# Performance work log

Measured on AMD Instinct MI355X. Metric: run time of the kernel, lower is better.

Reference implementation:

```python
import jax, jax.numpy as jnp
import numpy as np

N_NODES = 50000
N_EDGES = 800000
N_GRAPHS = 1024
N_PAIRS = 16384
N_CL = 16
IN_CH = 64
EMB = 128
HID = 256
OUT = 1


def _xavier(key, shape):
    fan_in, fan_out = shape[-2], shape[-1]
    lim = (6.0 / (fan_in + fan_out)) ** 0.5
    return jax.random.uniform(key, shape, jnp.float32, -lim, lim)


def setup_inputs() -> dict:
    key = jax.random.key(0)
    ks = jax.random.split(key, 12)
    x = jax.random.normal(ks[0], (N_NODES, IN_CH), jnp.float32)
    edge_index = jax.random.randint(ks[1], (2, N_EDGES), 0, N_NODES)
    batch = jnp.sort(jax.random.randint(ks[2], (N_NODES,), 0, N_GRAPHS))
    drug_drug_batch = jax.random.randint(ks[3], (2, N_PAIRS), 0, N_GRAPHS)
    edge_cell_lines = jax.random.randint(ks[4], (N_PAIRS,), 0, N_CL)
    conv1_w = _xavier(ks[5], (IN_CH, EMB))
    conv2_w = _xavier(ks[6], (EMB, EMB))
    reg_w1 = _xavier(ks[7], (N_CL, 2 * EMB, HID))
    reg_w2 = _xavier(ks[8], (N_CL, HID, OUT))
    return dict(
        x=x,
        conv1_w=conv1_w, conv1_b=jnp.zeros((EMB,), jnp.float32),
        conv2_w=conv2_w, conv2_b=jnp.zeros((EMB,), jnp.float32),
        reg_w1=reg_w1, reg_b1=jnp.zeros((N_CL, HID), jnp.float32),
        reg_w2=reg_w2, reg_b2=jnp.zeros((N_CL, OUT), jnp.float32),
        edge_index=edge_index, batch=batch,
        drug_drug_batch=drug_drug_batch, edge_cell_lines=edge_cell_lines,
    )


def _forward(x, conv1_w, conv1_b, conv2_w, conv2_b,
             reg_w1, reg_b1, reg_w2, reg_b2,
             edge_index, batch, drug_drug_batch, edge_cell_lines):
    n = x.shape[0]
    # GCN normalization with self-loops (PyG GCNConv default)
    loop = jnp.arange(n)
    row = jnp.concatenate([edge_index[0], loop])  # source
    col = jnp.concatenate([edge_index[1], loop])  # target
    deg = jax.ops.segment_sum(jnp.ones(row.shape[0], x.dtype), col, num_segments=n)
    dinv = jnp.where(deg > 0, jax.lax.rsqrt(deg), 0.0)
    norm = dinv[row] * dinv[col]  # [E+N]

    def gcn(h, W, b):
        hw = h @ W
        agg = jax.ops.segment_sum(norm[:, None] * hw[row], col, num_segments=n)
        return agg + b

    h = jax.nn.relu(gcn(x, conv1_w, conv1_b))
    h = jax.nn.relu(gcn(h, conv2_w, conv2_b))

    # scatter-mean pooling over graphs
    gsum = jax.ops.segment_sum(h, batch, num_segments=N_GRAPHS)
    cnt = jax.ops.segment_sum(jnp.ones(n, h.dtype), batch, num_segments=N_GRAPHS)
    graph_embeds = gsum / jnp.maximum(cnt, 1.0)[:, None]

    # np.digitize(ddb, unique(ddb)+1); with contiguous ids 0..G-1 this is identity,
    # expressed faithfully via searchsorted against bins = arange(G)+1
    bins = jnp.arange(N_GRAPHS) + 1
    q = jnp.searchsorted(bins, drug_drug_batch, side='right')
    pair = jnp.concatenate([graph_embeds[q[0]], graph_embeds[q[1]]], axis=1)  # [P, 2*EMB]

    # per-cell-line Linear-ReLU-Linear, computed for all lines then selected
    hcl = jax.nn.relu(jnp.einsum('pe,ceh->pch', pair, reg_w1) + reg_b1[None])  # [P,C,H]
    ocl = jnp.einsum('pch,cho->pco', hcl, reg_w2) + reg_b2[None]               # [P,C,O]
    preds = jnp.take_along_axis(ocl, edge_cell_lines[:, None, None], axis=1)[:, 0, :]
    return preds


def reference(x, conv1_w, conv1_b, conv2_w, conv2_b,
              reg_w1, reg_b1, reg_w2, reg_b2,
              edge_index, batch, drug_drug_batch, edge_cell_lines):
    return _forward(x, conv1_w, conv1_b, conv2_w, conv2_b,
                    reg_w1, reg_b1, reg_w2, reg_b2,
                    edge_index, batch, drug_drug_batch, edge_cell_lines)
```

## Files before the change

kernel.cpp:

```cpp
#include <hip/hip_runtime.h>
#include <hip/hip_fp16.h>

#define NN 50000
#define NE 800000
#define NG 1024
#define NP 16384
#define NCL 16
#define INCH 64
#define EMB 128
#define HID 256

#define NB 391
#define NCHUNK 400
#define EPB 2000

#define CDIV(a,b) (((a)+(b)-1)/(b))

typedef _Float16 f16x8 __attribute__((ext_vector_type(8)));
typedef float    f32x4 __attribute__((ext_vector_type(4)));

template<int NW>
__device__ __forceinline__ int block_excl_scan(int v, int t, int* incl_out) {
    int lane = t & 63, w = t >> 6;
    int s = v;
#pragma unroll
    for (int d = 1; d < 64; d <<= 1) {
        int u = __shfl_up(s, d, 64);
        if (lane >= d) s += u;
    }
    __shared__ int wsum[NW];
    if (lane == 63) wsum[w] = s;
    __syncthreads();
    int add = 0;
    for (int k = 0; k < w; ++k) add += wsum[k];
    *incl_out = s + add;
    return s + add - v;
}

__global__ __launch_bounds__(256) void k_cnt(const int* __restrict__ cols,
                                             int* __restrict__ cnt) {
    __shared__ int hist[NB];
    int ch = blockIdx.x, t = threadIdx.x;
    for (int b = t; b < NB; b += 256) hist[b] = 0;
    __syncthreads();
    for (int e = ch * EPB + t; e < (ch + 1) * EPB; e += 256)
        atomicAdd(&hist[cols[e] >> 7], 1);
    __syncthreads();
    for (int b = t; b < NB; b += 256) cnt[b * NCHUNK + ch] = hist[b];
}

__global__ __launch_bounds__(512) void k_bscan(int* __restrict__ cnt,
                                               int* __restrict__ btot) {
    int b = blockIdx.x, t = threadIdx.x;
    int v = (t < NCHUNK) ? cnt[b * NCHUNK + t] : 0;
    int incl;
    int excl = block_excl_scan<8>(v, t, &incl);
    if (t < NCHUNK) cnt[b * NCHUNK + t] = excl;
    if (t == NCHUNK - 1) btot[b] = incl;
}

__global__ __launch_bounds__(512) void k_btot(const int* __restrict__ btot,
                                              int* __restrict__ bbase) {
    int t = threadIdx.x;
    int v = (t < NB) ? btot[t] : 0;
    int incl;
    int excl = block_excl_scan<8>(v, t, &incl);
    if (t < NB) bbase[t] = excl;
    if (t == NB - 1) bbase[NB] = incl;
}

__global__ __launch_bounds__(256) void k_part(const int* __restrict__ rows,
                                              const int* __restrict__ cols,
                                              const int* __restrict__ cnt,
                                              const int* __restrict__ bbase,
                                              int* __restrict__ ebuf) {
    __shared__ int cur[NB];
    int ch = blockIdx.x, t = threadIdx.x;
    for (int b = t; b < NB; b += 256) cur[b] = bbase[b] + cnt[b * NCHUNK + ch];
    __syncthreads();
    for (int e = ch * EPB + t; e < (ch + 1) * EPB; e += 256) {
        int c = cols[e], r = rows[e];
        int pos = atomicAdd(&cur[c >> 7], 1);
        ebuf[pos] = (r << 7) | (c & 127);
    }
}

__global__ __launch_bounds__(256) void k_bsort(const int* __restrict__ ebuf,
                                               const int* __restrict__ bbase,
                                               const float* __restrict__ x,
                                               int* __restrict__ off,
                                               float* __restrict__ dinv,
                                               int* __restrict__ srows,
                                               __half* __restrict__ xs) {
    __shared__ int   ldeg[128];
    __shared__ int   lcur[128];
    __shared__ float ldinv[128];
    int b = blockIdx.x, t = threadIdx.x;
    int n0 = b << 7;
    int nloc = min(128, NN - n0);
    int beg = bbase[b], end = bbase[b + 1];
    if (t < 128) ldeg[t] = 0;
    __syncthreads();
    for (int i = beg + t; i < end; i += 256)
        atomicAdd(&ldeg[ebuf[i] & 127], 1);
    __syncthreads();
    int v = (t < nloc) ? ldeg[t] : 0;
    int incl;
    int excl = block_excl_scan<4>(v, t, &incl);
    if (t < nloc) {
        off[n0 + t]  = beg + excl + v;
        float d = rsqrtf((float)(v + 1));
        dinv[n0 + t] = d;
        ldinv[t] = d;
        lcur[t] = beg + excl;
    }
    __syncthreads();
    for (int i = beg + t; i < end; i += 256) {
        int e = ebuf[i];
        int pos = atomicAdd(&lcur[e & 127], 1);
        srows[pos] = e >> 7;
    }
    const float4* Xx = (const float4*)x;
#pragma unroll
    for (int i = 0; i < 8; ++i) {
        int f4 = t + i * 256;
        int rloc = f4 >> 4, kq = f4 & 15;
        if (rloc < nloc) {
            float d = ldinv[rloc];
            float4 vv = Xx[(size_t)(n0 + rloc) * 16 + kq];
            __half2 h[2];
            h[0] = __floats2half2_rn(d * vv.x, d * vv.y);
            h[1] = __floats2half2_rn(d * vv.z, d * vv.w);
            ((float2*)xs)[(size_t)(n0 + rloc) * 16 + kq] = *(float2*)h;
        }
    }
}

__global__ __launch_bounds__(256) void k_wconv(const float* __restrict__ W,
                                               __half* __restrict__ WT, int K) {
    int i = blockIdx.x * 256 + threadIdx.x;
    if (i >= K * 128) return;
    int k = i >> 7, n = i & 127;
    WT[n * K + k] = __float2half(W[i]);
}

template<int FEAT, bool ZB>
__global__ __launch_bounds__(256) void k_gath_h(const int* __restrict__ off,
                                                const int* __restrict__ srows,
                                                const float* __restrict__ dinv,
                                                const __half* __restrict__ SRC,
                                                __half* __restrict__ DST,
                                                float* __restrict__ zbuf) {
    if (ZB) {
        if (blockIdx.x < 512) zbuf[(blockIdx.x << 8) + threadIdx.x] = 0.f;
    }
    constexpr int NC = FEAT / 8;
    constexpr int PL = NC / 8;
    int node = blockIdx.x * 4 + (threadIdx.x >> 6);
    int lane = threadIdx.x & 63;
    int slot = lane >> 3, q = lane & 7;
    if (node >= NN) return;
    int beg = node ? off[node - 1] : 0;
    int end = off[node];
    float di = dinv[node];
    const float4* S4 = (const float4*)SRC;

    float acc[PL][8];
#pragma unroll
    for (int i = 0; i < PL; ++i)
#pragma unroll
        for (int j = 0; j < 8; ++j) acc[i][j] = 0.f;

    if (slot == 0) {
#pragma unroll
        for (int i = 0; i < PL; ++i) {
            float4 raw = S4[node * NC + i * 8 + q];
            const __half2* h = (const __half2*)&raw;
#pragma unroll
            for (int j = 0; j < 4; ++j) {
                float2 f = __half22float2(h[j]);
                acc[i][2 * j + 0] = f.x;
                acc[i][2 * j + 1] = f.y;
            }
        }
    }
    for (int e = beg + slot; e < end; e += 8) {
        int r = srows[e];
#pragma unroll
        for (int i = 0; i < PL; ++i) {
            float4 raw = S4[r * NC + i * 8 + q];
            const __half2* h = (const __half2*)&raw;
#pragma unroll
            for (int j = 0; j < 4; ++j) {
                float2 f = __half22float2(h[j]);
                acc[i][2 * j + 0] += f.x;
                acc[i][2 * j + 1] += f.y;
            }
        }
    }
#pragma unroll
    for (int d = 8; d < 64; d <<= 1)
#pragma unroll
        for (int i = 0; i < PL; ++i)
#pragma unroll
            for (int j = 0; j < 8; ++j)
                acc[i][j] += __shfl_xor(acc[i][j], d, 64);

    if (lane < 8) {
        float4* D4 = (float4*)DST;
#pragma unroll
        for (int i = 0; i < PL; ++i) {
            float4 pk;
            __half2* hp = (__half2*)&pk;
            hp[0] = __floats2half2_rn(di * acc[i][0], di * acc[i][1]);
            hp[1] = __floats2half2_rn(di * acc[i][2], di * acc[i][3]);
            hp[2] = __floats2half2_rn(di * acc[i][4], di * acc[i][5]);
            hp[3] = __floats2half2_rn(di * acc[i][6], di * acc[i][7]);
            D4[node * NC + i * 8 + lane] = pk;
        }
    }
}

template<int K, bool RS, bool POOL>
__global__ __launch_bounds__(256) void gemm_mf(const __half* __restrict__ X,
                                               const __half* __restrict__ WT,
                                               const float* __restrict__ bias,
                                               const float* __restrict__ rs,
                                               const int* __restrict__ batch,
                                               float* __restrict__ Y, int M) {
    constexpr int KP = K + 8;
    __shared__ __half Xs[64 * KP];
    __shared__ __half Ws[128 * KP];
    __shared__ int sb[64];
    const int t = threadIdx.x;
    const int row0 = blockIdx.x * 64;

    const float4* X8 = (const float4*)X;
#pragma unroll
    for (int i = t; i < 64 * (K / 8); i += 256) {
        int r = i / (K / 8), ch = i % (K / 8);
        float4 v = make_float4(0.f, 0.f, 0.f, 0.f);
        if (row0 + r < M) v = X8[(size_t)(row0 + r) * (K / 8) + ch];
        *(float4*)&Xs[r * KP + ch * 8] = v;
    }
    const float4* W8 = (const float4*)WT;
#pragma unroll
    for (int i = t; i < 128 * (K / 8); i += 256) {
        int n = i / (K / 8), ch = i % (K / 8);
        *(float4*)&Ws[n * KP + ch * 8] = W8[i];
    }
    if (POOL) {
        if (t < 64) sb[t] = (row0 + t < M) ? batch[row0 + t] : -1;
    }
    __syncthreads();

    const int w  = t >> 6;
    const int l  = t & 63;
    const int lm = l & 15, lg = l >> 4;

    f32x4 acc[8];
#pragma unroll
    for (int c = 0; c < 8; ++c) acc[c] = (f32x4){0.f, 0.f, 0.f, 0.f};

#pragma unroll
    for (int kk = 0; kk < K / 32; ++kk) {
        f16x8 a = *(const f16x8*)&Xs[(16 * w + lm) * KP + kk * 32 + lg * 8];
#pragma unroll
        for (int c = 0; c < 8; ++c) {
            f16x8 bf = *(const f16x8*)&Ws[(16 * c + lm) * KP + kk * 32 + lg * 8];
            acc[c] = __builtin_amdgcn_mfma_f32_16x16x32_f16(a, bf, acc[c], 0, 0, 0);
        }
    }

    float bcol[8];
#pragma unroll
    for (int c = 0; c < 8; ++c) bcol[c] = bias[16 * c + lm];

    if (POOL) {
#pragma unroll
        for (int c = 0; c < 8; ++c) {
            int rung = -1;
            float run = 0.f;
#pragma unroll
            for (int j = 0; j < 4; ++j) {
                int rr = 16 * w + 4 * lg + j;
                int g = (row0 + rr < M) ? sb[rr] : -1;
                if (g != rung) {
                    if (rung >= 0) atomicAdd(&Y[rung * 128 + 16 * c + lm], run);
                    run = 0.f;
                    rung = g;
                }
                if (g >= 0) run += fmaxf(acc[c][j] + bcol[c], 0.f);
            }
            if (rung >= 0) atomicAdd(&Y[rung * 128 + 16 * c + lm], run);
        }
        return;
    }

    __half* Yh = (__half*)Y;
#pragma unroll
    for (int j = 0; j < 4; ++j) {
        int r = row0 + 16 * w + 4 * lg + j;
        if (r < M) {
            float d = RS ? rs[r] : 1.f;
#pragma unroll
            for (int c = 0; c < 8; ++c) {
                float v = d * fmaxf(acc[c][j] + bcol[c], 0.f);
                Yh[(size_t)r * 128 + 16 * c + lm] = __float2half(v);
            }
        }
    }
}

__global__ __launch_bounds__(128) void k_div(float* __restrict__ gsum,
                                             const int* __restrict__ batch) {
    int g = blockIdx.x;
    __shared__ float inv;
    if (threadIdx.x == 0) {
        int lo = 0, hi = NN;
        while (lo < hi) { int m = (lo + hi) >> 1; if (batch[m] < g) lo = m + 1; else hi = m; }
        int s = lo;
        lo = 0; hi = NN;
        while (lo < hi) { int m = (lo + hi) >> 1; if (batch[m] < g + 1) lo = m + 1; else hi = m; }
        float c = (float)(lo - s);
        inv = 1.f / fmaxf(c, 1.f);
    }
    __syncthreads();
    gsum[g * 128 + threadIdx.x] *= inv;
}

__global__ __launch_bounds__(256) void gemm_bat(const float* __restrict__ GE,
                                                const float* __restrict__ W1,
                                                float* __restrict__ Aarr,
                                                float* __restrict__ Barr) {
    __shared__ float Xt[32][132];
    __shared__ float Wsh[32][128];
    const int t  = threadIdx.x;
    const int tr = t >> 4;
    const int tc = t & 15;
    const int row0 = blockIdx.x * 128;
    const int y = blockIdx.y;
    const int z = blockIdx.z;
    const int lrow = t & 127;
    const int khalf = t >> 7;

    const float* Wbase = W1 + (z >> 1) * (HID * HID) + (z & 1) * (128 * HID) + y * 128;

    float acc[8][8];
#pragma unroll
    for (int i = 0; i < 8; ++i)
#pragma unroll
        for (int j = 0; j < 8; ++j) acc[i][j] = 0.f;

    const float4* X4 = (const float4*)GE;

    for (int k0 = 0; k0 < 128; k0 += 32) {
        __syncthreads();
#pragma unroll
        for (int q = 0; q < 4; ++q) {
            int kq = 4 * khalf + q;
            float4 xv = X4[(row0 + lrow) * 32 + (k0 >> 2) + kq];
            Xt[4 * kq + 0][lrow] = xv.x;
            Xt[4 * kq + 1][lrow] = xv.y;
            Xt[4 * kq + 2][lrow] = xv.z;
            Xt[4 * kq + 3][lrow] = xv.w;
        }
        const float4* Wc4 = (const float4*)(Wbase + k0 * HID);
#pragma unroll
        for (int i = 0; i < 4; ++i) {
            int f4 = t + i * 256;
            int k = f4 >> 5, c4 = f4 & 31;
            ((float4*)&Wsh[k][0])[c4] = Wc4[k * 64 + c4];
        }
        __syncthreads();
#pragma unroll 2
        for (int k = 0; k < 32; ++k) {
            float xf[8], wf[8];
            *(float4*)&xf[0] = *(const float4*)&Xt[k][8 * tr];
            *(float4*)&xf[4] = *(const float4*)&Xt[k][8 * tr + 4];
            *(float4*)&wf[0] = *(const float4*)&Wsh[k][8 * tc];
            *(float4*)&wf[4] = *(const float4*)&Wsh[k][8 * tc + 4];
#pragma unroll
            for (int i = 0; i < 8; ++i)
#pragma unroll
                for (int j = 0; j < 8; ++j)
                    acc[i][j] = fmaf(xf[i], wf[j], acc[i][j]);
        }
    }
    float* Obase = (z & 1) ? Barr : Aarr;
    float4* O4 = (float4*)Obase;
#pragma unroll
    for (int i = 0; i < 8; ++i) {
        int g = row0 + 8 * tr + i;
        size_t base = ((size_t)((z >> 1) * NG + g) * HID + y * 128 + 8 * tc) >> 2;
        O4[base + 0] = make_float4(acc[i][0], acc[i][1], acc[i][2], acc[i][3]);
        O4[base + 1] = make_float4(acc[i][4], acc[i][5], acc[i][6], acc[i][7]);
    }
}

__global__ __launch_bounds__(256) void k_pair(const float* __restrict__ Aarr,
                                              const float* __restrict__ Barr,
                                              const int* __restrict__ ddb,
                                              const int* __restrict__ ecl,
                                              const float* __restrict__ B1,
                                              const float* __restrict__ W2,
                                              const float* __restrict__ B2,
                                              float* __restrict__ out) {
    int p = blockIdx.x * 4 + (threadIdx.x >> 6);
    int lane = threadIdx.x & 63;
    int c = ecl[p];
    int a = ddb[p];
    int b = ddb[NP + p];
    const float4* rA = (const float4*)&Aarr[((size_t)c * NG + a) * HID];
    const float4* rB = (const float4*)&Barr[((size_t)c * NG + b) * HID];
    const float4* b1 = (const float4*)&B1[c * HID];
    const float4* w2 = (const float4*)&W2[c * HID];
    float4 va = rA[lane], vb = rB[lane], v1 = b1[lane], v2 = w2[lane];
    float hx = va.x + vb.x + v1.x;
    float hy = va.y + vb.y + v1.y;
    float hz = va.z + vb.z + v1.z;
    float hw = va.w + vb.w + v1.w;
    float s = 0.f;
    s = fmaf(hx > 0.f ? hx : 0.f, v2.x, s);
    s = fmaf(hy > 0.f ? hy : 0.f, v2.y, s);
    s = fmaf(hz > 0.f ? hz : 0.f, v2.z, s);
    s = fmaf(hw > 0.f ? hw : 0.f, v2.w, s);
    for (int o = 32; o; o >>= 1) s += __shfl_down(s, o, 64);
    if (lane == 0) out[p] = s + B2[c];
}

extern "C" void kernel_launch(void* const* d_in, const int* in_sizes, int n_in,
                              void* d_out, int out_size, void* d_ws, size_t ws_size,
                              hipStream_t stream) {
    const float* x    = (const float*)d_in[0];
    const float* c1w  = (const float*)d_in[1];
    const float* c1b  = (const float*)d_in[2];
    const float* c2w  = (const float*)d_in[3];
    const float* c2b  = (const float*)d_in[4];
    const float* rw1  = (const float*)d_in[5];
    const float* rb1  = (const float*)d_in[6];
    const float* rw2  = (const float*)d_in[7];
    const float* rb2  = (const float*)d_in[8];
    const int*   eidx = (const int*)d_in[9];
    const int*   batch= (const int*)d_in[10];
    const int*   ddb  = (const int*)d_in[11];
    const int*   ecl  = (const int*)d_in[12];
    float* out = (float*)d_out;

    int*   off   = (int*)d_ws;
    int*   srows = off + 50048;
    float* dinv  = (float*)(srows + NE);
    float* bufA  = dinv + 50048;
    float* bufB  = bufA + NN * EMB;

    int*    ebuf  = (int*)bufA;
    int*    cnt   = (int*)(bufB + 1700000);
    int*    btot  = cnt + NB * NCHUNK;
    int*    bbase = btot + 512;
    __half* xs    = (__half*)bufB;
    __half* aggXh = (__half*)bufA;
    __half* H1h   = (__half*)bufB;
    __half* aggHh = (__half*)bufA;
    float*  gsum  = bufA + 4500000;
    __half* w1t   = (__half*)(bufA + 4700000);
    __half* w2t   = (__half*)(bufA + 4710000);
    float*  Aarr  = bufA;
    float*  Barr  = bufB;

    const int* erow = eidx;
    const int* ecol = eidx + NE;

    k_wconv<<<CDIV(INCH*128,256),256,0,stream>>>(c1w, w1t, INCH);
    k_wconv<<<CDIV(EMB*128,256),256,0,stream>>>(c2w, w2t, EMB);

    k_cnt  <<<NCHUNK, 256, 0, stream>>>(ecol, cnt);
    k_bscan<<<NB,     512, 0, stream>>>(cnt, btot);
    k_btot <<<1,      512, 0, stream>>>(btot, bbase);
    k_part <<<NCHUNK, 256, 0, stream>>>(erow, ecol, cnt, bbase, ebuf);
    k_bsort<<<NB,     256, 0, stream>>>(ebuf, bbase, x, off, dinv, srows, xs);

    k_gath_h<INCH,true><<<CDIV(NN,4),256,0,stream>>>(off, srows, dinv, xs, aggXh, gsum);
    gemm_mf<INCH,true,false><<<CDIV(NN,64),256,0,stream>>>(aggXh, w1t, c1b, dinv, nullptr, (float*)H1h, NN);

    k_gath_h<EMB,false><<<CDIV(NN,4),256,0,stream>>>(off, srows, dinv, H1h, aggHh, nullptr);
    gemm_mf<EMB,false,true><<<CDIV(NN,64),256,0,stream>>>(aggHh, w2t, c2b, nullptr, batch, gsum, NN);
    k_div<<<NG,128,0,stream>>>(gsum, batch);

    dim3 bgrid(NG/128, 2, 2*NCL);
    gemm_bat<<<bgrid,256,0,stream>>>(gsum, rw1, Aarr, Barr);
    k_pair<<<NP/4,256,0,stream>>>(Aarr, Barr, ddb, ecl, rb1, rw2, rb2, out);
}
```

Before: 178.3 us.

## Move per-cell-line pair GEMM to fp16 MFMA with hi/lo split weights

Replaces the fp32 FMA batched GEMM (graph embeddings x regressor W1) with an MFMA 16x16x32 fp16 kernel. The weights are pre-split into hi and lo fp16 halves by a new conversion kernel and accumulated in two passes to recover precision. The graph-mean kernel now emits fp16 embeddings. Embeddings are rounded to fp16 without compensation, and an extra weight-conversion kernel runs on every call.

```diff
diff --git a/kernel.cpp b/kernel.cpp
--- a/kernel.cpp
+++ b/kernel.cpp
@@ -144,6 +144,25 @@
     WT[n * K + k] = __float2half(W[i]);
 }
 
+__global__ __launch_bounds__(256) void k_wconvb(const float* __restrict__ W1,
+                                                __half* __restrict__ Whl) {
+    int i = blockIdx.x * 256 + threadIdx.x;
+    if (i >= 32 * 256 * 16) return;
+    int ch = i & 15, tg = (i >> 4) & 255, z = i >> 12;
+    int c = z >> 1, part = z & 1;
+    f16x8 hi, lo;
+#pragma unroll
+    for (int j = 0; j < 8; ++j) {
+        float v = W1[(size_t)c * 65536 + (size_t)(part * 128 + ch * 8 + j) * 256 + tg];
+        _Float16 h = (_Float16)v;
+        hi[j] = h;
+        lo[j] = (_Float16)(v - (float)h);
+    }
+    size_t base = ((size_t)z * 256 + tg) * 16 + ch;
+    ((f16x8*)Whl)[base] = hi;
+    ((f16x8*)Whl)[(size_t)32 * 256 * 16 + base] = lo;
+}
+
 template<int FEAT, bool ZB>
 __global__ __launch_bounds__(256) void k_gath_h(const int* __restrict__ off,
                                                 const int* __restrict__ srows,
@@ -312,8 +331,9 @@
     }
 }
 
-__global__ __launch_bounds__(128) void k_div(float* __restrict__ gsum,
-                                             const int* __restrict__ batch) {
+__global__ __launch_bounds__(128) void k_div(const float* __restrict__ gsum,
+                                             const int* __restrict__ batch,
+                                             __half* __restrict__ geh) {
     int g = blockIdx.x;
     __shared__ float inv;
     if (threadIdx.x == 0) {
@@ -326,75 +346,65 @@
         inv = 1.f / fmaxf(c, 1.f);
     }
     __syncthreads();
-    gsum[g * 128 + threadIdx.x] *= inv;
-}
-
-__global__ __launch_bounds__(256) void gemm_bat(const float* __restrict__ GE,
-                                                const float* __restrict__ W1,
+    geh[g * 128 + threadIdx.x] = __float2half(gsum[g * 128 + threadIdx.x] * inv);
+}
+
+__global__ __launch_bounds__(256) void gemm_bat(const __half* __restrict__ GEh,
+                                                const __half* __restrict__ Whl,
                                                 float* __restrict__ Aarr,
                                                 float* __restrict__ Barr) {
-    __shared__ float Xt[32][132];
-    __shared__ float Wsh[32][128];
-    const int t  = threadIdx.x;
-    const int tr = t >> 4;
-    const int tc = t & 15;
-    const int row0 = blockIdx.x * 128;
-    const int y = blockIdx.y;
-    const int z = blockIdx.z;
-    const int lrow = t & 127;
-    const int khalf = t >> 7;
-
-    const float* Wbase = W1 + (z >> 1) * (HID * HID) + (z & 1) * (128 * HID) + y * 128;
-
-    float acc[8][8];
-#pragma unroll
-    for (int i = 0; i < 8; ++i)
-#pragma unroll
-        for (int j = 0; j < 8; ++j) acc[i][j] = 0.f;
-
-    const float4* X4 = (const float4*)GE;
-
-    for (int k0 = 0; k0 < 128; k0 += 32) {
+    constexpr int KP = 128 + 8;
+    __shared__ __half Xs[64 * KP];
+    __shared__ __half Ws[128 * KP];
+    const int t = threadIdx.x;
+    const int row0 = blockIdx.x * 64;
+    const int y = blockIdx.y, z = blockIdx.z;
+
+    const float4* X8 = (const float4*)GEh;
+#pragma unroll
+    for (int i = t; i < 64 * 16; i += 256) {
+        int r = i >> 4, ch = i & 15;
+        *(float4*)&Xs[r * KP + ch * 8] = X8[(size_t)(row0 + r) * 16 + ch];
+    }
+
+    const int w  = t >> 6;
+    const int l  = t & 63;
+    const int lm = l & 15, lg = l >> 4;
+
+    f32x4 acc[8];
+#pragma unroll
+    for (int c = 0; c < 8; ++c) acc[c] = (f32x4){0.f, 0.f, 0.f, 0.f};
+
+    const float4* W8 = (const float4*)Whl;
+#pragma unroll
+    for (int pass = 0; pass < 2; ++pass) {
         __syncthreads();
-#pragma unroll
-        for (int q = 0; q < 4; ++q) {
-            int kq = 4 * khalf + q;
-            float4 xv = X4[(row0 + lrow) * 32 + (k0 >> 2) + kq];
-            Xt[4 * kq + 0][lrow] = xv.x;
-            Xt[4 * kq + 1][lrow] = xv.y;
-            Xt[4 * kq + 2][lrow] = xv.z;
-            Xt[4 * kq + 3][lrow] = xv.w;
-        }
-        const float4* Wc4 = (const float4*)(Wbase + k0 * HID);
-#pragma unroll
-        for (int i = 0; i < 4; ++i) {
-            int f4 = t + i * 256;
-            int k = f4 >> 5, c4 = f4 & 31;
-            ((float4*)&Wsh[k][0])[c4] = Wc4[k * 64 + c4];
+        size_t wbase = ((size_t)pass * 32 + z) * 256 * 16;
+#pragma unroll
+        for (int i = t; i < 128 * 16; i += 256) {
+            int n = i >> 4, ch = i & 15;
+            *(float4*)&Ws[n * KP + ch * 8] = W8[wbase + (size_t)(y * 128 + n) * 16 + ch];
         }
         __syncthreads();
-#pragma unroll 2
-        for (int k = 0; k < 32; ++k) {
-            float xf[8], wf[8];
-            *(float4*)&xf[0] = *(const float4*)&Xt[k][8 * tr];
-            *(float4*)&xf[4] = *(const float4*)&Xt[k][8 * tr + 4];
-            *(float4*)&wf[0] = *(const float4*)&Wsh[k][8 * tc];
-            *(float4*)&wf[4] = *(const float4*)&Wsh[k][8 * tc + 4];
-#pragma unroll
-            for (int i = 0; i < 8; ++i)
-#pragma unroll
-                for (int j = 0; j < 8; ++j)
-                    acc[i][j] = fmaf(xf[i], wf[j], acc[i][j]);
-        }
-    }
+#pragma unroll
+        for (int kk = 0; kk < 4; ++kk) {
+            f16x8 a = *(const f16x8*)&Xs[(16 * w + lm) * KP + kk * 32 + lg * 8];
+#pragma unroll
+            for (int c = 0; c < 8; ++c) {
+                f16x8 bf = *(const f16x8*)&Ws[(16 * c + lm) * KP + kk * 32 + lg * 8];
+                acc[c] = __builtin_amdgcn_mfma_f32_16x16x32_f16(a, bf, acc[c], 0, 0, 0);
+            }
+        }
+    }
+
     float* Obase = (z & 1) ? Barr : Aarr;
-    float4* O4 = (float4*)Obase;
-#pragma unroll
-    for (int i = 0; i < 8; ++i) {
-        int g = row0 + 8 * tr + i;
-        size_t base = ((size_t)((z >> 1) * NG + g) * HID + y * 128 + 8 * tc) >> 2;
-        O4[base + 0] = make_float4(acc[i][0], acc[i][1], acc[i][2], acc[i][3]);
-        O4[base + 1] = make_float4(acc[i][4], acc[i][5], acc[i][6], acc[i][7]);
+#pragma unroll
+    for (int j = 0; j < 4; ++j) {
+        int g = row0 + 16 * w + 4 * lg + j;
+        size_t rb = ((size_t)(z >> 1) * NG + g) * HID + y * 128;
+#pragma unroll
+        for (int c = 0; c < 8; ++c)
+            Obase[rb + 16 * c + lm] = acc[c][j];
     }
 }
 
@@ -464,6 +474,8 @@
     float*  gsum  = bufA + 4500000;
     __half* w1t   = (__half*)(bufA + 4700000);
     __half* w2t   = (__half*)(bufA + 4710000);
+    __half* geh   = (__half*)(bufA + 4720000);
+    __half* Whl   = (__half*)(bufB + 4300000);
     float*  Aarr  = bufA;
     float*  Barr  = bufB;
 
@@ -472,6 +484,7 @@
 
     k_wconv<<<CDIV(INCH*128,256),256,0,stream>>>(c1w, w1t, INCH);
     k_wconv<<<CDIV(EMB*128,256),256,0,stream>>>(c2w, w2t, EMB);
+    k_wconvb<<<CDIV(32*256*16,256),256,0,stream>>>(rw1, Whl);
 
     k_cnt  <<<NCHUNK, 256, 0, stream>>>(ecol, cnt);
     k_bscan<<<NB,     512, 0, stream>>>(cnt, btot);
@@ -484,9 +497,9 @@
 
     k_gath_h<EMB,false><<<CDIV(NN,4),256,0,stream>>>(off, srows, dinv, H1h, aggHh, nullptr);
     gemm_mf<EMB,false,true><<<CDIV(NN,64),256,0,stream>>>(aggHh, w2t, c2b, nullptr, batch, gsum, NN);
-    k_div<<<NG,128,0,stream>>>(gsum, batch);
-
-    dim3 bgrid(NG/128, 2, 2*NCL);
-    gemm_bat<<<bgrid,256,0,stream>>>(gsum, rw1, Aarr, Barr);
+    k_div<<<NG,128,0,stream>>>(gsum, batch, geh);
+
+    dim3 bgrid(NG/64, 2, 2*NCL);
+    gemm_bat<<<bgrid,256,0,stream>>>(geh, Whl, Aarr, Barr);
     k_pair<<<NP/4,256,0,stream>>>(Aarr, Barr, ddb, ecl, rb1, rw2, rb2, out);
 }
```

New measurement: 171.9 us. 1.04x faster.
